# Kernel tuning notes

Measured on AMD Instinct MI355X. Metric: run time of the kernel, lower is better.

## Reference

```python
import jax, jax.numpy as jnp
import numpy as np

V, D, U, B, S = 100000, 256, 512, 64, 128


def setup_inputs() -> dict:
    key = jax.random.key(0)
    k0, k1, k2, k3 = jax.random.split(key, 4)
    x = jax.random.randint(k0, (B, S), 0, V)  # token ids
    hidden = jnp.zeros((B, U), jnp.float32)   # initialize_hidden_state()
    embedding = jax.random.normal(k1, (V, D), jnp.float32) * 0.02
    kernel = jax.random.normal(k2, (D, 3 * U), jnp.float32) * (1.0 / np.sqrt(D))
    recurrent_kernel = jax.random.normal(k3, (U, 3 * U), jnp.float32) * (1.0 / np.sqrt(U))
    bias = jnp.zeros((2, 3 * U), jnp.float32)  # [input_bias, recurrent_bias] (reset_after=True)
    return {"x": x, "hidden": hidden, "embedding": embedding,
            "kernel": kernel, "recurrent_kernel": recurrent_kernel, "bias": bias}


def reference(x, hidden, embedding, kernel, recurrent_kernel, bias):
    # Vectorized replacement of the token-by-token get_embedding gather.
    emb = embedding[x]                      # [B, S, D]
    b_in, b_rec = bias[0], bias[1]
    # Precompute all input projections in one GEMM: [B, S, 3U]
    xp = jnp.einsum('bsd,dk->bsk', emb, kernel) + b_in

    def step(h, xt):
        rp = h @ recurrent_kernel + b_rec           # [B, 3U]
        xz, xr, xh = jnp.split(xt, 3, axis=-1)
        rz, rr, rh = jnp.split(rp, 3, axis=-1)
        z = jax.nn.sigmoid(xz + rz)
        r = jax.nn.sigmoid(xr + rr)
        hh = jnp.tanh(xh + r * rh)                  # reset_after=True form
        hn = z * h + (1.0 - z) * hh
        return hn, hn

    state, outs = jax.lax.scan(step, hidden, jnp.swapaxes(xp, 0, 1))
    output = jnp.swapaxes(outs, 0, 1)               # [B, S, U]
    return output, state
```

## Files before the change

### kernel.cpp

```cpp
#include <hip/hip_runtime.h>
#include <hip/hip_bf16.h>

#define NB   64
#define NS   128
#define ND   256
#define NU   512
#define N3   1536

typedef __attribute__((ext_vector_type(4))) float  f32x4;
typedef __attribute__((ext_vector_type(8))) short  s16x8;
typedef unsigned long long u64;
typedef unsigned int       u32;
typedef unsigned short     u16;

#define SENT64  0x7FC07FC07FC07FC0ull
#define BIT14x4 0x4000400040004000ull

__device__ __forceinline__ u16 f2bf(float v) {
  unsigned u = __builtin_bit_cast(unsigned, v);
  u += 0x7fffu + ((u >> 16) & 1u);
  return (u16)(u >> 16);
}

__global__ __launch_bounds__(512) void init_kernel(const float* __restrict__ hidden,
                                                   u16* __restrict__ hx) {
  const int tid = blockIdx.x * 512 + threadIdx.x;
  hx[tid] = f2bf(hidden[tid]);
  u64* fill = (u64*)(hx + NB * NU);
  const int n = 127 * NB * NU / 4;
  for (int i = tid; i < n; i += NB * NU) fill[i] = SENT64;
}

__global__ __launch_bounds__(256) void xproj_kernel(
    const int* __restrict__ x, const float* __restrict__ emb,
    const float* __restrict__ W, const float* __restrict__ bias,
    float* __restrict__ xp) {
  __shared__ float As[32][68];
  __shared__ float Bs[32][68];
  __shared__ int tok[64];
  const int tid = threadIdx.x;
  const int m0 = blockIdx.y * 64;
  const int n0 = blockIdx.x * 64;
  if (tid < 64) tok[tid] = x[m0 + tid];
  __syncthreads();
  const int tx = tid & 15, ty = tid >> 4;
  float acc[4][4] = {};
  for (int k0 = 0; k0 < ND; k0 += 32) {
    {
      const int m = tid & 63, kq = tid >> 6;
      const float* src = emb + (size_t)tok[m] * ND + k0 + kq * 8;
      const float4 v0 = *(const float4*)(src);
      const float4 v1 = *(const float4*)(src + 4);
      As[kq*8+0][m] = v0.x; As[kq*8+1][m] = v0.y;
      As[kq*8+2][m] = v0.z; As[kq*8+3][m] = v0.w;
      As[kq*8+4][m] = v1.x; As[kq*8+5][m] = v1.y;
      As[kq*8+6][m] = v1.z; As[kq*8+7][m] = v1.w;
    }
    {
      const int n = (tid & 15) * 4, k = tid >> 4;
      *(float4*)&Bs[k][n]    = *(const float4*)&W[(size_t)(k0 + k) * N3 + n0 + n];
      *(float4*)&Bs[k+16][n] = *(const float4*)&W[(size_t)(k0 + k + 16) * N3 + n0 + n];
    }
    __syncthreads();
    #pragma unroll
    for (int kk = 0; kk < 32; ++kk) {
      const float4 b4 = *(const float4*)&Bs[kk][tx * 4];
      float a[4];
      #pragma unroll
      for (int i = 0; i < 4; ++i) a[i] = As[kk][ty * 4 + i];
      #pragma unroll
      for (int i = 0; i < 4; ++i) {
        acc[i][0] += a[i] * b4.x;
        acc[i][1] += a[i] * b4.y;
        acc[i][2] += a[i] * b4.z;
        acc[i][3] += a[i] * b4.w;
      }
    }
    __syncthreads();
  }
  #pragma unroll
  for (int i = 0; i < 4; ++i) {
    const size_t row = (size_t)(m0 + ty * 4 + i) * N3 + n0 + tx * 4;
    float4 o;
    o.x = acc[i][0] + bias[n0 + tx*4 + 0];
    o.y = acc[i][1] + bias[n0 + tx*4 + 1];
    o.z = acc[i][2] + bias[n0 + tx*4 + 2];
    o.w = acc[i][3] + bias[n0 + tx*4 + 3];
    *(float4*)&xp[row] = o;
  }
}

__global__ __launch_bounds__(128) void gru_scan_kernel(
    const float* __restrict__ xp, const float* __restrict__ hidden,
    const float* __restrict__ R, const float* __restrict__ bias,
    float* __restrict__ out, u16* __restrict__ hx) {
  __shared__ u16 Rt[96][520];

  const int bid = blockIdx.x;
  const int g   = bid >> 4;
  const int u0  = (bid & 15) * 32;
  const int tid = threadIdx.x;
  const int lane = tid & 63;
  const int wv   = tid >> 6;

  for (int idx = tid; idx < 512 * 128; idx += 128) {
    const int k = idx >> 7, c = idx & 127;
    if (c < 96) {
      const int wc = c / 48, r = c % 48, j = r >> 4, cuu = r & 15;
      Rt[c][k] = f2bf(R[(size_t)k * N3 + (j << 9) + u0 + (wc << 4) + cuu]);
    }
  }
  __syncthreads();

  const int ar  = lane & 15;
  const int kg  = lane >> 4;
  const int cu  = lane & 15;
  const int myu = u0 + (wv << 4) + cu;
  const int drow = kg << 2;
  const int cb  = wv * 48 + cu;

  const float bz = bias[N3 + myu];
  const float br = bias[N3 + 512 + myu];
  const float bh = bias[N3 + 1024 + myu];

  float hr[4];
  #pragma unroll
  for (int i = 0; i < 4; ++i)
    hr[i] = hidden[(size_t)((g << 4) + drow + i) * NU + myu];

  for (int t = 0; t < NS; ++t) {
    float xg0[4], xg1[4], xg2[4];
    #pragma unroll
    for (int i = 0; i < 4; ++i) {
      const float* q = xp + ((size_t)(((g << 4) + drow + i) * NS) + t) * N3 + myu;
      xg0[i] = q[0]; xg1[i] = q[512]; xg2[i] = q[1024];
    }

    u64 alo[16], ahi[16];
    const u64* hrow = (const u64*)(hx + ((size_t)t * NB + (g << 4) + ar) * NU);
    int ok = 0;
    do {
      if (!ok) {
        #pragma unroll
        for (int ks = 0; ks < 16; ++ks) {
          const int qi = (ks << 3) + (kg << 1);
          alo[ks] = __hip_atomic_load(&hrow[qi],     __ATOMIC_RELAXED, __HIP_MEMORY_SCOPE_AGENT);
          ahi[ks] = __hip_atomic_load(&hrow[qi + 1], __ATOMIC_RELAXED, __HIP_MEMORY_SCOPE_AGENT);
        }
        u64 m = 0;
        #pragma unroll
        for (int ks = 0; ks < 16; ++ks) m |= alo[ks] | ahi[ks];
        ok = ((m & BIT14x4) == 0) ? 1 : 0;
      }
    } while (!__all(ok));

    f32x4 a0 = {0.f,0.f,0.f,0.f}, a1 = a0, a2 = a0;
    #pragma unroll
    for (int ks = 0; ks < 16; ++ks) {
      union { u64 q[2]; s16x8 v; } af;
      af.q[0] = alo[ks]; af.q[1] = ahi[ks];
      const int kb = (ks << 5) + (kg << 3);
      a0 = __builtin_amdgcn_mfma_f32_16x16x32_bf16(af.v, *(const s16x8*)&Rt[cb][kb],      a0, 0,0,0);
      a1 = __builtin_amdgcn_mfma_f32_16x16x32_bf16(af.v, *(const s16x8*)&Rt[cb + 16][kb], a1, 0,0,0);
      a2 = __builtin_amdgcn_mfma_f32_16x16x32_bf16(af.v, *(const s16x8*)&Rt[cb + 32][kb], a2, 0,0,0);
    }

    #pragma unroll
    for (int i = 0; i < 4; ++i) {
      const float z = 1.f / (1.f + __expf(-(xg0[i] + a0[i] + bz)));
      const float r = 1.f / (1.f + __expf(-(xg1[i] + a1[i] + br)));
      const float e = __expf(2.f * (xg2[i] + r * (a2[i] + bh)));
      const float hh = 1.f - 2.f / (e + 1.f);
      hr[i] = z * hr[i] + (1.f - z) * hh;
    }

    if (t < NS - 1) {
      #pragma unroll
      for (int i = 0; i < 4; ++i)
        __hip_atomic_store(&hx[((size_t)(t + 1) * NB + (g << 4) + drow + i) * NU + myu],
                           f2bf(hr[i]), __ATOMIC_RELAXED, __HIP_MEMORY_SCOPE_AGENT);
    }

    #pragma unroll
    for (int i = 0; i < 4; ++i)
      out[((size_t)((g << 4) + drow + i) * NS + t) * NU + myu] = hr[i];
    if (t == NS - 1) {
      #pragma unroll
      for (int i = 0; i < 4; ++i)
        out[(size_t)NB * NS * NU + (size_t)((g << 4) + drow + i) * NU + myu] = hr[i];
    }
  }
}

extern "C" void kernel_launch(void* const* d_in, const int* in_sizes, int n_in,
                              void* d_out, int out_size, void* d_ws, size_t ws_size,
                              hipStream_t stream) {
  const int*   x      = (const int*)d_in[0];
  const float* hidden = (const float*)d_in[1];
  const float* emb    = (const float*)d_in[2];
  const float* W      = (const float*)d_in[3];
  const float* R      = (const float*)d_in[4];
  const float* bias   = (const float*)d_in[5];
  float* out = (float*)d_out;

  char* ws = (char*)d_ws;
  float* xp  = (float*)ws;
  u16*   hx  = (u16*)(ws + 50331648);

  init_kernel<<<NB, NU, 0, stream>>>(hidden, hx);
  dim3 gA(N3 / 64, (NB * NS) / 64);
  xproj_kernel<<<gA, 256, 0, stream>>>(x, emb, W, bias, xp);
  gru_scan_kernel<<<64, 128, 0, stream>>>(xp, hidden, R, bias, out, hx);
}
```

Baseline: 825.7 us.

## Run four batch groups per GRU block with register-resident weights and prefetch

The recurrent scan now uses 16 blocks instead of 64. Each block handles all four 16-row batch groups in turn, keeping its recurrent-weight fragments in registers instead of re-reading LDS every step. While one group runs its MFMAs and gate math, the next group's hidden-state slab and input projections are already being loaded, hiding the sentinel-poll and global-load latency behind compute. In exchange there are 4x fewer parallel blocks, heavy register pressure (48 B fragments plus two 32-entry slab buffers), and the per-step work of each block is serialized across groups.

New measurement: 2.948 ms. 257% more time.

```diff
diff --git a/kernel.cpp b/kernel.cpp
--- a/kernel.cpp
+++ b/kernel.cpp
@@ -90,15 +90,82 @@
   }
 }
 
-__global__ __launch_bounds__(128) void gru_scan_kernel(
+
+#define LOADSLABS(BUF_, G_, T_) do {                                            \
+    const u64* hq_ = (const u64*)(hx + ((size_t)(T_) * NB + ((G_) << 4) + ar) * NU); \
+    _Pragma("unroll")                                                           \
+    for (int ks_ = 0; ks_ < 16; ++ks_) {                                        \
+      BUF_[2*ks_]   = __hip_atomic_load(&hq_[ks_*8 + kg*2],                     \
+                        __ATOMIC_RELAXED, __HIP_MEMORY_SCOPE_AGENT);            \
+      BUF_[2*ks_+1] = __hip_atomic_load(&hq_[ks_*8 + kg*2 + 1],                 \
+                        __ATOMIC_RELAXED, __HIP_MEMORY_SCOPE_AGENT);            \
+    }                                                                           \
+  } while (0)
+
+#define LOADXP(XZ_, XR_, XH_, G_, T_) do {                                      \
+    _Pragma("unroll")                                                           \
+    for (int i_ = 0; i_ < 4; ++i_) {                                            \
+      const float* q_ = xp + ((size_t)((((G_) << 4) + drow + i_) * NS) + (T_)) * N3 + myu; \
+      XZ_[i_] = q_[0]; XR_[i_] = q_[512]; XH_[i_] = q_[1024];                   \
+    }                                                                           \
+  } while (0)
+
+#define PHASE(T_, G_, CUR_, NXT_, XZC_, XRC_, XHC_, XZN_, XRN_, XHN_, GN_, TN_) do { \
+    LOADSLABS(NXT_, GN_, TN_);                 \
+    LOADXP(XZN_, XRN_, XHN_, GN_, TN_);        \
+    { u64 m_ = 0;                                                               \
+      _Pragma("unroll") for (int q_ = 0; q_ < 32; ++q_) m_ |= CUR_[q_];         \
+      int ok_ = ((m_ & BIT14x4) == 0) ? 1 : 0;                                  \
+      while (!__all(ok_)) {                                                     \
+        if (!ok_) {                                                             \
+          LOADSLABS(CUR_, G_, T_);                                              \
+          m_ = 0;                                                               \
+          _Pragma("unroll") for (int q_ = 0; q_ < 32; ++q_) m_ |= CUR_[q_];     \
+          ok_ = ((m_ & BIT14x4) == 0) ? 1 : 0;                                  \
+        }                                                                       \
+      }                                                                         \
+    }                                                                           \
+    f32x4 a0_ = {0.f,0.f,0.f,0.f}, a1_ = a0_, a2_ = a0_;                        \
+    _Pragma("unroll")                                                           \
+    for (int ks_ = 0; ks_ < 16; ++ks_) {                                        \
+      union { u64 q[2]; s16x8 v; } af_;                                         \
+      af_.q[0] = CUR_[2*ks_]; af_.q[1] = CUR_[2*ks_+1];                         \
+      a0_ = __builtin_amdgcn_mfma_f32_16x16x32_bf16(af_.v, bfr[ks_],      a0_, 0,0,0); \
+      a1_ = __builtin_amdgcn_mfma_f32_16x16x32_bf16(af_.v, bfr[16 + ks_], a1_, 0,0,0); \
+      a2_ = __builtin_amdgcn_mfma_f32_16x16x32_bf16(af_.v, bfr[32 + ks_], a2_, 0,0,0); \
+    }                                                                           \
+    _Pragma("unroll")                                                           \
+    for (int i_ = 0; i_ < 4; ++i_) {                                            \
+      const float z_ = 1.f / (1.f + __expf(-(XZC_[i_] + a0_[i_] + bz)));        \
+      const float r_ = 1.f / (1.f + __expf(-(XRC_[i_] + a1_[i_] + br)));        \
+      const float e_ = __expf(2.f * (XHC_[i_] + r_ * (a2_[i_] + bh)));          \
+      const float hh_ = 1.f - 2.f / (e_ + 1.f);        \
+      hr[G_][i_] = z_ * hr[G_][i_] + (1.f - z_) * hh_;                          \
+    }                                                                           \
+    if ((T_) < NS - 1) {                                                        \
+      _Pragma("unroll")                                                         \
+      for (int i_ = 0; i_ < 4; ++i_)                                            \
+        __hip_atomic_store(&hx[((size_t)((T_) + 1) * NB + ((G_) << 4) + drow + i_) * NU + myu], \
+                           f2bf(hr[G_][i_]), __ATOMIC_RELAXED, __HIP_MEMORY_SCOPE_AGENT); \
+    }                                                                           \
+    _Pragma("unroll")                                                           \
+    for (int i_ = 0; i_ < 4; ++i_)                                              \
+      out[((size_t)(((G_) << 4) + drow + i_) * NS + (T_)) * NU + myu] = hr[G_][i_]; \
+    if ((T_) == NS - 1) {                                                       \
+      _Pragma("unroll")                                                         \
+      for (int i_ = 0; i_ < 4; ++i_)                                            \
+        out[(size_t)NB * NS * NU + (size_t)(((G_) << 4) + drow + i_) * NU + myu] = hr[G_][i_]; \
+    }                                                                           \
+  } while (0)
+
+__global__ __launch_bounds__(128, 1) void gru_scan_kernel(
     const float* __restrict__ xp, const float* __restrict__ hidden,
     const float* __restrict__ R, const float* __restrict__ bias,
     float* __restrict__ out, u16* __restrict__ hx) {
   __shared__ u16 Rt[96][520];
 
   const int bid = blockIdx.x;
-  const int g   = bid >> 4;
-  const int u0  = (bid & 15) * 32;
+  const int u0  = bid * 32;
   const int tid = threadIdx.x;
   const int lane = tid & 63;
   const int wv   = tid >> 6;
@@ -119,76 +186,35 @@
   const int drow = kg << 2;
   const int cb  = wv * 48 + cu;
 
+  s16x8 bfr[48];
+  #pragma unroll
+  for (int j = 0; j < 3; ++j)
+    #pragma unroll
+    for (int ks = 0; ks < 16; ++ks)
+      bfr[j * 16 + ks] = *(const s16x8*)&Rt[cb + 16 * j][ks * 32 + kg * 8];
+
   const float bz = bias[N3 + myu];
   const float br = bias[N3 + 512 + myu];
   const float bh = bias[N3 + 1024 + myu];
 
-  float hr[4];
+  float hr[4][4];
   #pragma unroll
-  for (int i = 0; i < 4; ++i)
-    hr[i] = hidden[(size_t)((g << 4) + drow + i) * NU + myu];
-
-  for (int t = 0; t < NS; ++t) {
-    float xg0[4], xg1[4], xg2[4];
-    #pragma unroll
-    for (int i = 0; i < 4; ++i) {
-      const float* q = xp + ((size_t)(((g << 4) + drow + i) * NS) + t) * N3 + myu;
-      xg0[i] = q[0]; xg1[i] = q[512]; xg2[i] = q[1024];
-    }
-
-    u64 alo[16], ahi[16];
-    const u64* hrow = (const u64*)(hx + ((size_t)t * NB + (g << 4) + ar) * NU);
-    int ok = 0;
-    do {
-      if (!ok) {
-        #pragma unroll
-        for (int ks = 0; ks < 16; ++ks) {
-          const int qi = (ks << 3) + (kg << 1);
-          alo[ks] = __hip_atomic_load(&hrow[qi],     __ATOMIC_RELAXED, __HIP_MEMORY_SCOPE_AGENT);
-          ahi[ks] = __hip_atomic_load(&hrow[qi + 1], __ATOMIC_RELAXED, __HIP_MEMORY_SCOPE_AGENT);
-        }
-        u64 m = 0;
-        #pragma unroll
-        for (int ks = 0; ks < 16; ++ks) m |= alo[ks] | ahi[ks];
-        ok = ((m & BIT14x4) == 0) ? 1 : 0;
-      }
-    } while (!__all(ok));
-
-    f32x4 a0 = {0.f,0.f,0.f,0.f}, a1 = a0, a2 = a0;
-    #pragma unroll
-    for (int ks = 0; ks < 16; ++ks) {
-      union { u64 q[2]; s16x8 v; } af;
-      af.q[0] = alo[ks]; af.q[1] = ahi[ks];
-      const int kb = (ks << 5) + (kg << 3);
-      a0 = __builtin_amdgcn_mfma_f32_16x16x32_bf16(af.v, *(const s16x8*)&Rt[cb][kb],      a0, 0,0,0);
-      a1 = __builtin_amdgcn_mfma_f32_16x16x32_bf16(af.v, *(const s16x8*)&Rt[cb + 16][kb], a1, 0,0,0);
-      a2 = __builtin_amdgcn_mfma_f32_16x16x32_bf16(af.v, *(const s16x8*)&Rt[cb + 32][kb], a2, 0,0,0);
-    }
-
-    #pragma unroll
-    for (int i = 0; i < 4; ++i) {
-      const float z = 1.f / (1.f + __expf(-(xg0[i] + a0[i] + bz)));
-      const float r = 1.f / (1.f + __expf(-(xg1[i] + a1[i] + br)));
-      const float e = __expf(2.f * (xg2[i] + r * (a2[i] + bh)));
-      const float hh = 1.f - 2.f / (e + 1.f);
-      hr[i] = z * hr[i] + (1.f - z) * hh;
-    }
-
-    if (t < NS - 1) {
-      #pragma unroll
-      for (int i = 0; i < 4; ++i)
-        __hip_atomic_store(&hx[((size_t)(t + 1) * NB + (g << 4) + drow + i) * NU + myu],
-                           f2bf(hr[i]), __ATOMIC_RELAXED, __HIP_MEMORY_SCOPE_AGENT);
-    }
-
+  for (int G = 0; G < 4; ++G)
     #pragma unroll
     for (int i = 0; i < 4; ++i)
-      out[((size_t)((g << 4) + drow + i) * NS + t) * NU + myu] = hr[i];
-    if (t == NS - 1) {
-      #pragma unroll
-      for (int i = 0; i < 4; ++i)
-        out[(size_t)NB * NS * NU + (size_t)((g << 4) + drow + i) * NU + myu] = hr[i];
-    }
+      hr[G][i] = hidden[(size_t)((G << 4) + drow + i) * NU + myu];
+
+  u64 s0[32], s1[32];
+  float xz0[4], xr0[4], xh0[4], xz1[4], xr1[4], xh1[4];
+  LOADSLABS(s0, 0, 0);
+  LOADXP(xz0, xr0, xh0, 0, 0);
+
+  for (int t = 0; t < NS; ++t) {
+    const int tn = (t + 1 < NS) ? t + 1 : 0;
+    PHASE(t, 0, s0, s1, xz0, xr0, xh0, xz1, xr1, xh1, 1, t);
+    PHASE(t, 1, s1, s0, xz1, xr1, xh1, xz0, xr0, xh0, 2, t);
+    PHASE(t, 2, s0, s1, xz0, xr0, xh0, xz1, xr1, xh1, 3, t);
+    PHASE(t, 3, s1, s0, xz1, xr1, xh1, xz0, xr0, xh0, 0, tn);
   }
 }
 
@@ -210,5 +236,5 @@
   init_kernel<<<NB, NU, 0, stream>>>(hidden, hx);
   dim3 gA(N3 / 64, (NB * NS) / 64);
   xproj_kernel<<<gA, 256, 0, stream>>>(x, emb, W, bias, xp);
-  gru_scan_kernel<<<64, 128, 0, stream>>>(xp, hidden, R, bias, out, hx);
-}
+  gru_scan_kernel<<<16, 128, 0, stream>>>(xp, hidden, R, bias, out, hx);
+}
```

## Split GRU scan into 8-row batch groups over 128 blocks with sc0 polling

Applied to the files above, without the earlier changes.

Doubles the scan grid to 128 blocks, each owning 8 batch rows instead of 16. The MFMA A-tile is padded by duplicating rows, and only half the lanes compute gates. The spin-wait now polls with inline-asm dwordx4 loads using the sc0 cache bit for a fixed number of rounds, then falls back to sleeping atomic loads. Stores are issued with sc0 as well as atomically, so the next step's data becomes visible sooner. This shortens the per-step critical path and spreads the work over more CUs, at the cost of wasted MFMA work, duplicate stores and more polling traffic.

Measured after the change: 1.437 ms. 1.74x slower.

```diff
diff --git a/kernel.cpp b/kernel.cpp
--- a/kernel.cpp
+++ b/kernel.cpp
@@ -6,21 +6,47 @@
 #define ND   256
 #define NU   512
 #define N3   1536
+#define KFAST 8
 
 typedef __attribute__((ext_vector_type(4))) float  f32x4;
 typedef __attribute__((ext_vector_type(8))) short  s16x8;
+typedef __attribute__((ext_vector_type(4))) unsigned int u32x4;
 typedef unsigned long long u64;
 typedef unsigned int       u32;
 typedef unsigned short     u16;
 
-#define SENT64  0x7FC07FC07FC07FC0ull
-#define BIT14x4 0x4000400040004000ull
+#define SENT64   0x7FC07FC07FC07FC0ull
+#define BIT14x2  0x40004000u
 
 __device__ __forceinline__ u16 f2bf(float v) {
   unsigned u = __builtin_bit_cast(unsigned, v);
   u += 0x7fffu + ((u >> 16) & 1u);
   return (u16)(u >> 16);
 }
+
+#define LD16_SC0(dst, a, off)                                                   \
+  asm volatile("global_load_dwordx4 %0, %1, off offset:" #off " sc0"            \
+               : "=v"(dst) : "v"(a))
+
+#define ISSUE_SLABS(SL_, A_) do {                                               \
+    LD16_SC0(SL_[0],  A_, 0);    LD16_SC0(SL_[1],  A_, 64);                     \
+    LD16_SC0(SL_[2],  A_, 128);  LD16_SC0(SL_[3],  A_, 192);                    \
+    LD16_SC0(SL_[4],  A_, 256);  LD16_SC0(SL_[5],  A_, 320);                    \
+    LD16_SC0(SL_[6],  A_, 384);  LD16_SC0(SL_[7],  A_, 448);                    \
+    LD16_SC0(SL_[8],  A_, 512);  LD16_SC0(SL_[9],  A_, 576);                    \
+    LD16_SC0(SL_[10], A_, 640);  LD16_SC0(SL_[11], A_, 704);                    \
+    LD16_SC0(SL_[12], A_, 768);  LD16_SC0(SL_[13], A_, 832);                    \
+    LD16_SC0(SL_[14], A_, 896);  LD16_SC0(SL_[15], A_, 960);                    \
+    asm volatile("s_waitcnt vmcnt(0)" ::: "memory");                            \
+    __builtin_amdgcn_sched_barrier(0);                                          \
+  } while (0)
+
+#define ORMASK(M_, SL_) do {                                                    \
+    M_ = 0;                                                                     \
+    _Pragma("unroll")                                                           \
+    for (int q_ = 0; q_ < 16; ++q_)                                             \
+      M_ |= SL_[q_][0] | SL_[q_][1] | SL_[q_][2] | SL_[q_][3];                  \
+  } while (0)
 
 __global__ __launch_bounds__(512) void init_kernel(const float* __restrict__ hidden,
                                                    u16* __restrict__ hx) {
@@ -90,15 +116,15 @@
   }
 }
 
-__global__ __launch_bounds__(128) void gru_scan_kernel(
+__global__ __launch_bounds__(128, 1) void gru_scan_kernel(
     const float* __restrict__ xp, const float* __restrict__ hidden,
     const float* __restrict__ R, const float* __restrict__ bias,
     float* __restrict__ out, u16* __restrict__ hx) {
   __shared__ u16 Rt[96][520];
 
   const int bid = blockIdx.x;
-  const int g   = bid >> 4;
-  const int u0  = (bid & 15) * 32;
+  const int g   = bid & 7;
+  const int u0  = (bid >> 3) * 32;
   const int tid = threadIdx.x;
   const int lane = tid & 63;
   const int wv   = tid >> 6;
@@ -112,82 +138,99 @@
   }
   __syncthreads();
 
-  const int ar  = lane & 15;
+  const int ar8 = lane & 7;
   const int kg  = lane >> 4;
   const int cu  = lane & 15;
   const int myu = u0 + (wv << 4) + cu;
   const int drow = kg << 2;
   const int cb  = wv * 48 + cu;
+  const int gateln = (kg < 2);
 
   const float bz = bias[N3 + myu];
   const float br = bias[N3 + 512 + myu];
   const float bh = bias[N3 + 1024 + myu];
 
-  float hr[4];
-  #pragma unroll
-  for (int i = 0; i < 4; ++i)
-    hr[i] = hidden[(size_t)((g << 4) + drow + i) * NU + myu];
+  float hr[4] = {0.f, 0.f, 0.f, 0.f};
+  if (gateln) {
+    #pragma unroll
+    for (int i = 0; i < 4; ++i)
+      hr[i] = hidden[(size_t)(g * 8 + drow + i) * NU + myu];
+  }
 
   for (int t = 0; t < NS; ++t) {
-    float xg0[4], xg1[4], xg2[4];
-    #pragma unroll
-    for (int i = 0; i < 4; ++i) {
-      const float* q = xp + ((size_t)(((g << 4) + drow + i) * NS) + t) * N3 + myu;
-      xg0[i] = q[0]; xg1[i] = q[512]; xg2[i] = q[1024];
-    }
-
-    u64 alo[16], ahi[16];
-    const u64* hrow = (const u64*)(hx + ((size_t)t * NB + (g << 4) + ar) * NU);
-    int ok = 0;
-    do {
-      if (!ok) {
+    float xz[4], xr[4], xh[4];
+    if (gateln) {
+      #pragma unroll
+      for (int i = 0; i < 4; ++i) {
+        const float* q = xp + ((size_t)((g * 8 + drow + i) * NS) + t) * N3 + myu;
+        xz[i] = q[0]; xr[i] = q[512]; xh[i] = q[1024];
+      }
+    }
+
+    u32x4 sl[16];
+    const u64 abase = (u64)((const char*)(hx + ((size_t)t * NB + g * 8 + ar8) * NU)
+                            + kg * 16);
+    int done = 0;
+    for (int rnd = 0; rnd < KFAST; ++rnd) {
+      ISSUE_SLABS(sl, abase);
+      u32 m; ORMASK(m, sl);
+      done = __all(((m & BIT14x2) == 0) ? 1 : 0) ? 1 : 0;
+      if (done) break;
+    }
+    if (!done) {
+      const u64* hq = (const u64*)abase;
+      while (!done) {
+        __builtin_amdgcn_s_sleep(1);
         #pragma unroll
         for (int ks = 0; ks < 16; ++ks) {
-          const int qi = (ks << 3) + (kg << 1);
-          alo[ks] = __hip_atomic_load(&hrow[qi],     __ATOMIC_RELAXED, __HIP_MEMORY_SCOPE_AGENT);
-          ahi[ks] = __hip_atomic_load(&hrow[qi + 1], __ATOMIC_RELAXED, __HIP_MEMORY_SCOPE_AGENT);
+          union { u64 q[2]; u32x4 v; } w;
+          w.q[0] = __hip_atomic_load(&hq[ks * 8],     __ATOMIC_RELAXED, __HIP_MEMORY_SCOPE_AGENT);
+          w.q[1] = __hip_atomic_load(&hq[ks * 8 + 1], __ATOMIC_RELAXED, __HIP_MEMORY_SCOPE_AGENT);
+          sl[ks] = w.v;
         }
-        u64 m = 0;
-        #pragma unroll
-        for (int ks = 0; ks < 16; ++ks) m |= alo[ks] | ahi[ks];
-        ok = ((m & BIT14x4) == 0) ? 1 : 0;
-      }
-    } while (!__all(ok));
+        u32 m; ORMASK(m, sl);
+        done = __all(((m & BIT14x2) == 0) ? 1 : 0) ? 1 : 0;
+      }
+    }
 
     f32x4 a0 = {0.f,0.f,0.f,0.f}, a1 = a0, a2 = a0;
     #pragma unroll
     for (int ks = 0; ks < 16; ++ks) {
-      union { u64 q[2]; s16x8 v; } af;
-      af.q[0] = alo[ks]; af.q[1] = ahi[ks];
+      const s16x8 af = __builtin_bit_cast(s16x8, sl[ks]);
       const int kb = (ks << 5) + (kg << 3);
-      a0 = __builtin_amdgcn_mfma_f32_16x16x32_bf16(af.v, *(const s16x8*)&Rt[cb][kb],      a0, 0,0,0);
-      a1 = __builtin_amdgcn_mfma_f32_16x16x32_bf16(af.v, *(const s16x8*)&Rt[cb + 16][kb], a1, 0,0,0);
-      a2 = __builtin_amdgcn_mfma_f32_16x16x32_bf16(af.v, *(const s16x8*)&Rt[cb + 32][kb], a2, 0,0,0);
-    }
-
-    #pragma unroll
-    for (int i = 0; i < 4; ++i) {
-      const float z = 1.f / (1.f + __expf(-(xg0[i] + a0[i] + bz)));
-      const float r = 1.f / (1.f + __expf(-(xg1[i] + a1[i] + br)));
-      const float e = __expf(2.f * (xg2[i] + r * (a2[i] + bh)));
-      const float hh = 1.f - 2.f / (e + 1.f);
-      hr[i] = z * hr[i] + (1.f - z) * hh;
-    }
-
-    if (t < NS - 1) {
+      a0 = __builtin_amdgcn_mfma_f32_16x16x32_bf16(af, *(const s16x8*)&Rt[cb][kb],      a0, 0,0,0);
+      a1 = __builtin_amdgcn_mfma_f32_16x16x32_bf16(af, *(const s16x8*)&Rt[cb + 16][kb], a1, 0,0,0);
+      a2 = __builtin_amdgcn_mfma_f32_16x16x32_bf16(af, *(const s16x8*)&Rt[cb + 32][kb], a2, 0,0,0);
+    }
+
+    if (gateln) {
+      #pragma unroll
+      for (int i = 0; i < 4; ++i) {
+        const float z = 1.f / (1.f + __expf(-(xz[i] + a0[i] + bz)));
+        const float r = 1.f / (1.f + __expf(-(xr[i] + a1[i] + br)));
+        const float e = __expf(2.f * (xh[i] + r * (a2[i] + bh)));
+        const float hh = 1.f - 2.f / (e + 1.f);
+        hr[i] = z * hr[i] + (1.f - z) * hh;
+      }
+      if (t < NS - 1) {
+        #pragma unroll
+        for (int i = 0; i < 4; ++i) {
+          u16* dst = &hx[((size_t)(t + 1) * NB + g * 8 + drow + i) * NU + myu];
+          const u32 dv = (u32)f2bf(hr[i]);
+          const u64 ad = (u64)dst;
+          asm volatile("global_store_short %0, %1, off sc0"
+                       :: "v"(ad), "v"(dv) : "memory");
+          __hip_atomic_store(dst, (u16)dv, __ATOMIC_RELAXED, __HIP_MEMORY_SCOPE_AGENT);
+        }
+      }
       #pragma unroll
       for (int i = 0; i < 4; ++i)
-        __hip_atomic_store(&hx[((size_t)(t + 1) * NB + (g << 4) + drow + i) * NU + myu],
-                           f2bf(hr[i]), __ATOMIC_RELAXED, __HIP_MEMORY_SCOPE_AGENT);
-    }
-
-    #pragma unroll
-    for (int i = 0; i < 4; ++i)
-      out[((size_t)((g << 4) + drow + i) * NS + t) * NU + myu] = hr[i];
-    if (t == NS - 1) {
-      #pragma unroll
-      for (int i = 0; i < 4; ++i)
-        out[(size_t)NB * NS * NU + (size_t)((g << 4) + drow + i) * NU + myu] = hr[i];
+        out[((size_t)(g * 8 + drow + i) * NS + t) * NU + myu] = hr[i];
+      if (t == NS - 1) {
+        #pragma unroll
+        for (int i = 0; i < 4; ++i)
+          out[(size_t)NB * NS * NU + (size_t)(g * 8 + drow + i) * NU + myu] = hr[i];
+      }
     }
   }
 }
@@ -204,11 +247,11 @@
   float* out = (float*)d_out;
 
   char* ws = (char*)d_ws;
-  float* xp  = (float*)ws;
-  u16*   hx  = (u16*)(ws + 50331648);
+  float* xp = (float*)ws;
+  u16*   hx = (u16*)(ws + 50331648);
 
   init_kernel<<<NB, NU, 0, stream>>>(hidden, hx);
   dim3 gA(N3 / 64, (NB * NS) / 64);
   xproj_kernel<<<gA, 256, 0, stream>>>(x, emb, W, bias, xp);
-  gru_scan_kernel<<<64, 128, 0, stream>>>(xp, hidden, R, bias, out, hx);
-}
+  gru_scan_kernel<<<128, 128, 0, stream>>>(xp, hidden, R, bias, out, hx);
+}
```

## Replace persistent spin-synchronized GRU scan with per-timestep kernel launches

Applied to the files above, without the earlier changes.

The persistent scan kernel, which spun on sentinel-tagged bf16 hidden states in global memory, is replaced by 128 separate step launches. Each launch reads the previous hidden state from ping-pong fp32 and bf16 buffers, and a new pre-pass writes a transposed bf16 copy of the recurrent weights. This removes the spin polling and the 24MB sentinel fill, and carries hidden state in fp32 rather than bf16. The cost is 128 kernel launch gaps and recurrent weights read from global/L2 on every step instead of sitting in shared memory.

Result: slower. 851.7 us (+3.2%).

```diff
diff --git a/kernel.cpp b/kernel.cpp
--- a/kernel.cpp
+++ b/kernel.cpp
@@ -13,22 +13,38 @@
 typedef unsigned int       u32;
 typedef unsigned short     u16;
 
-#define SENT64  0x7FC07FC07FC07FC0ull
-#define BIT14x4 0x4000400040004000ull
-
 __device__ __forceinline__ u16 f2bf(float v) {
   unsigned u = __builtin_bit_cast(unsigned, v);
   u += 0x7fffu + ((u >> 16) & 1u);
   return (u16)(u >> 16);
 }
 
-__global__ __launch_bounds__(512) void init_kernel(const float* __restrict__ hidden,
-                                                   u16* __restrict__ hx) {
+__global__ __launch_bounds__(512) void hinit_kernel(const float* __restrict__ hidden,
+                                                    float* __restrict__ hf,
+                                                    u16* __restrict__ hb) {
   const int tid = blockIdx.x * 512 + threadIdx.x;
-  hx[tid] = f2bf(hidden[tid]);
-  u64* fill = (u64*)(hx + NB * NU);
-  const int n = 127 * NB * NU / 4;
-  for (int i = tid; i < n; i += NB * NU) fill[i] = SENT64;
+  const float v = hidden[tid];
+  hf[tid] = v;
+  hb[tid] = f2bf(v);
+}
+
+__global__ __launch_bounds__(256) void rtrans_kernel(const float* __restrict__ R,
+                                                     u16* __restrict__ Rbf) {
+  __shared__ float ld[64][65];
+  const int c0 = blockIdx.x * 64;
+  const int k0 = blockIdx.y * 64;
+  const int tx = threadIdx.x & 63, ty = threadIdx.x >> 6;
+  #pragma unroll
+  for (int r = 0; r < 16; ++r) {
+    const int k = ty + r * 4;
+    ld[k][tx] = R[(size_t)(k0 + k) * N3 + c0 + tx];
+  }
+  __syncthreads();
+  #pragma unroll
+  for (int r = 0; r < 16; ++r) {
+    const int c = ty + r * 4;
+    Rbf[(size_t)(c0 + c) * NU + k0 + tx] = f2bf(ld[tx][c]);
+  }
 }
 
 __global__ __launch_bounds__(256) void xproj_kernel(
@@ -90,104 +106,71 @@
   }
 }
 
-__global__ __launch_bounds__(128) void gru_scan_kernel(
-    const float* __restrict__ xp, const float* __restrict__ hidden,
-    const float* __restrict__ R, const float* __restrict__ bias,
-    float* __restrict__ out, u16* __restrict__ hx) {
-  __shared__ u16 Rt[96][520];
-
+__global__ __launch_bounds__(128) void gru_step_kernel(
+    const float* __restrict__ xp, const u16* __restrict__ Rbf,
+    const float* __restrict__ bias,
+    const u16* __restrict__ hi16, const float* __restrict__ hi32,
+    u16* __restrict__ ho16, float* __restrict__ ho32,
+    float* __restrict__ out, int t) {
   const int bid = blockIdx.x;
   const int g   = bid >> 4;
   const int u0  = (bid & 15) * 32;
-  const int tid = threadIdx.x;
-  const int lane = tid & 63;
-  const int wv   = tid >> 6;
-
-  for (int idx = tid; idx < 512 * 128; idx += 128) {
-    const int k = idx >> 7, c = idx & 127;
-    if (c < 96) {
-      const int wc = c / 48, r = c % 48, j = r >> 4, cuu = r & 15;
-      Rt[c][k] = f2bf(R[(size_t)k * N3 + (j << 9) + u0 + (wc << 4) + cuu]);
-    }
-  }
-  __syncthreads();
+  const int lane = threadIdx.x & 63;
+  const int wv   = threadIdx.x >> 6;
 
   const int ar  = lane & 15;
   const int kg  = lane >> 4;
   const int cu  = lane & 15;
   const int myu = u0 + (wv << 4) + cu;
   const int drow = kg << 2;
-  const int cb  = wv * 48 + cu;
+
+  float xg0[4], xg1[4], xg2[4];
+  #pragma unroll
+  for (int i = 0; i < 4; ++i) {
+    const float* q = xp + ((size_t)(((g << 4) + drow + i) * NS) + t) * N3 + myu;
+    xg0[i] = q[0]; xg1[i] = q[512]; xg2[i] = q[1024];
+  }
+  float hp[4];
+  #pragma unroll
+  for (int i = 0; i < 4; ++i)
+    hp[i] = hi32[(size_t)((g << 4) + drow + i) * NU + myu];
+
+  const u16* ha = hi16 + ((size_t)(g << 4) + ar) * NU + (kg << 3);
+  s16x8 af[16];
+  #pragma unroll
+  for (int ks = 0; ks < 16; ++ks)
+    af[ks] = *(const s16x8*)(ha + (ks << 5));
+
+  const u16* b0 = Rbf + ((size_t)(       myu) << 9) + (kg << 3);
+  const u16* b1 = Rbf + ((size_t)( 512 + myu) << 9) + (kg << 3);
+  const u16* b2 = Rbf + ((size_t)(1024 + myu) << 9) + (kg << 3);
+
+  f32x4 a0 = {0.f,0.f,0.f,0.f}, a1 = a0, a2 = a0;
+  #pragma unroll
+  for (int ks = 0; ks < 16; ++ks) {
+    a0 = __builtin_amdgcn_mfma_f32_16x16x32_bf16(af[ks], *(const s16x8*)(b0 + (ks << 5)), a0, 0,0,0);
+    a1 = __builtin_amdgcn_mfma_f32_16x16x32_bf16(af[ks], *(const s16x8*)(b1 + (ks << 5)), a1, 0,0,0);
+    a2 = __builtin_amdgcn_mfma_f32_16x16x32_bf16(af[ks], *(const s16x8*)(b2 + (ks << 5)), a2, 0,0,0);
+  }
 
   const float bz = bias[N3 + myu];
   const float br = bias[N3 + 512 + myu];
   const float bh = bias[N3 + 1024 + myu];
 
-  float hr[4];
-  #pragma unroll
-  for (int i = 0; i < 4; ++i)
-    hr[i] = hidden[(size_t)((g << 4) + drow + i) * NU + myu];
-
-  for (int t = 0; t < NS; ++t) {
-    float xg0[4], xg1[4], xg2[4];
-    #pragma unroll
-    for (int i = 0; i < 4; ++i) {
-      const float* q = xp + ((size_t)(((g << 4) + drow + i) * NS) + t) * N3 + myu;
-      xg0[i] = q[0]; xg1[i] = q[512]; xg2[i] = q[1024];
-    }
-
-    u64 alo[16], ahi[16];
-    const u64* hrow = (const u64*)(hx + ((size_t)t * NB + (g << 4) + ar) * NU);
-    int ok = 0;
-    do {
-      if (!ok) {
-        #pragma unroll
-        for (int ks = 0; ks < 16; ++ks) {
-          const int qi = (ks << 3) + (kg << 1);
-          alo[ks] = __hip_atomic_load(&hrow[qi],     __ATOMIC_RELAXED, __HIP_MEMORY_SCOPE_AGENT);
-          ahi[ks] = __hip_atomic_load(&hrow[qi + 1], __ATOMIC_RELAXED, __HIP_MEMORY_SCOPE_AGENT);
-        }
-        u64 m = 0;
-        #pragma unroll
-        for (int ks = 0; ks < 16; ++ks) m |= alo[ks] | ahi[ks];
-        ok = ((m & BIT14x4) == 0) ? 1 : 0;
-      }
-    } while (!__all(ok));
-
-    f32x4 a0 = {0.f,0.f,0.f,0.f}, a1 = a0, a2 = a0;
-    #pragma unroll
-    for (int ks = 0; ks < 16; ++ks) {
-      union { u64 q[2]; s16x8 v; } af;
-      af.q[0] = alo[ks]; af.q[1] = ahi[ks];
-      const int kb = (ks << 5) + (kg << 3);
-      a0 = __builtin_amdgcn_mfma_f32_16x16x32_bf16(af.v, *(const s16x8*)&Rt[cb][kb],      a0, 0,0,0);
-      a1 = __builtin_amdgcn_mfma_f32_16x16x32_bf16(af.v, *(const s16x8*)&Rt[cb + 16][kb], a1, 0,0,0);
-      a2 = __builtin_amdgcn_mfma_f32_16x16x32_bf16(af.v, *(const s16x8*)&Rt[cb + 32][kb], a2, 0,0,0);
-    }
-
-    #pragma unroll
-    for (int i = 0; i < 4; ++i) {
-      const float z = 1.f / (1.f + __expf(-(xg0[i] + a0[i] + bz)));
-      const float r = 1.f / (1.f + __expf(-(xg1[i] + a1[i] + br)));
-      const float e = __expf(2.f * (xg2[i] + r * (a2[i] + bh)));
-      const float hh = 1.f - 2.f / (e + 1.f);
-      hr[i] = z * hr[i] + (1.f - z) * hh;
-    }
-
+  #pragma unroll
+  for (int i = 0; i < 4; ++i) {
+    const float z = 1.f / (1.f + __expf(-(xg0[i] + a0[i] + bz)));
+    const float r = 1.f / (1.f + __expf(-(xg1[i] + a1[i] + br)));
+    const float e = __expf(2.f * (xg2[i] + r * (a2[i] + bh)));
+    const float hh = (e - 1.f) / (e + 1.f);
+    const float hn = z * hp[i] + (1.f - z) * hh;
+    const size_t b = (size_t)(g << 4) + drow + i;
+    out[(b * NS + t) * NU + myu] = hn;
     if (t < NS - 1) {
-      #pragma unroll
-      for (int i = 0; i < 4; ++i)
-        __hip_atomic_store(&hx[((size_t)(t + 1) * NB + (g << 4) + drow + i) * NU + myu],
-                           f2bf(hr[i]), __ATOMIC_RELAXED, __HIP_MEMORY_SCOPE_AGENT);
-    }
-
-    #pragma unroll
-    for (int i = 0; i < 4; ++i)
-      out[((size_t)((g << 4) + drow + i) * NS + t) * NU + myu] = hr[i];
-    if (t == NS - 1) {
-      #pragma unroll
-      for (int i = 0; i < 4; ++i)
-        out[(size_t)NB * NS * NU + (size_t)((g << 4) + drow + i) * NU + myu] = hr[i];
+      ho32[b * NU + myu] = hn;
+      ho16[b * NU + myu] = f2bf(hn);
+    } else {
+      out[(size_t)NB * NS * NU + b * NU + myu] = hn;
     }
   }
 }
@@ -204,11 +187,23 @@
   float* out = (float*)d_out;
 
   char* ws = (char*)d_ws;
-  float* xp  = (float*)ws;
-  u16*   hx  = (u16*)(ws + 50331648);
-
-  init_kernel<<<NB, NU, 0, stream>>>(hidden, hx);
+  float* xp   = (float*)ws;
+  u16*   Rbf  = (u16*)(ws + 50331648);
+  u16*   hb16 = (u16*)(ws + 50331648 + 1572864);
+  float* hf32 = (float*)(ws + 50331648 + 1572864 + 131072);
+
+  hinit_kernel<<<NB, NU, 0, stream>>>(hidden, hf32, hb16);
+  dim3 gT(N3 / 64, NU / 64);
+  rtrans_kernel<<<gT, 256, 0, stream>>>(R, Rbf);
   dim3 gA(N3 / 64, (NB * NS) / 64);
   xproj_kernel<<<gA, 256, 0, stream>>>(x, emb, W, bias, xp);
-  gru_scan_kernel<<<64, 128, 0, stream>>>(xp, hidden, R, bias, out, hx);
-}
+
+  for (int t = 0; t < NS; ++t) {
+    const u16*   hi16 = hb16 + (t & 1) * (NB * NU);
+    u16*         ho16 = hb16 + ((t + 1) & 1) * (NB * NU);
+    const float* hi32 = hf32 + (t & 1) * (NB * NU);
+    float*       ho32 = hf32 + ((t + 1) & 1) * (NB * NU);
+    gru_step_kernel<<<64, 128, 0, stream>>>(xp, Rbf, bias, hi16, hi32,
+                                            ho16, ho32, out, t);
+  }
+}
```
